# Kernel tuning notes

Hardware: AMD Instinct MI355X
Metric: run time of the kernel (lower is better)

## Reference

```python
import jax, jax.numpy as jnp
import numpy as np

N, D, E, TOPK = 8192, 2048, 8, 2

def setup_inputs() -> dict:
    key = jax.random.key(0)
    k1, k2, k3, k4 = jax.random.split(key, 4)
    inputs = jax.random.normal(k1, (N, D), dtype=jnp.float32)
    Wg = jax.random.normal(k2, (D, E), dtype=jnp.float32) * 0.02
    We = jax.random.normal(k3, (E, D, D), dtype=jnp.float32) * 0.02
    be = jax.random.normal(k4, (E, D), dtype=jnp.float32) * 0.02
    return {"inputs": inputs, "Wg": Wg, "We": We, "be": be}

def reference(inputs, Wg, We, be):
    # gate: [N, E] logits, top-k routing, softmax over the k selected logits (in fp32)
    gate_logits = inputs @ Wg                      # [N, E]
    topk_vals, selected = jax.lax.top_k(gate_logits, TOPK)  # [N, K], [N, K]
    weights = jax.nn.softmax(topk_vals.astype(jnp.float32), axis=1).astype(inputs.dtype)  # [N, K]

    results = jnp.zeros_like(inputs)
    for i in range(E):
        # combine weight for expert i per token (0 if not routed to i)
        coeff = jnp.sum(jnp.where(selected == i, weights, 0.0), axis=1)  # [N]
        expert_out = inputs @ We[i] + be[i]        # [N, D]
        results = results + coeff[:, None] * expert_out
    return results
```

## Files before the change

kernel.cpp:

```cpp
#include <hip/hip_runtime.h>
#include <stdint.h>

typedef unsigned short u16;
typedef __bf16 bf16x8 __attribute__((ext_vector_type(8)));
typedef float  f32x4  __attribute__((ext_vector_type(4)));

#define N_TOK 8192
#define DIM   2048
#define NEXP  8
#define RPAD  18432
#define NCHUNK 32
#define GT    576

#define OFF_CNT   0
#define OFF_HIST  1024
#define OFF_PRE   2048
#define OFF_RE    4096
#define OFF_RI    (OFF_RE + N_TOK * 8)
#define OFF_RW    (OFF_RI + N_TOK * 16)
#define OFF_TIDX  (OFF_RW + N_TOK * 8)
#define OFF_XB    (OFF_TIDX + NEXP * N_TOK * 4)
#define OFF_WT    (OFF_XB + (size_t)N_TOK * DIM * 2)
#define OFF_YP    (OFF_WT + (size_t)NEXP * DIM * DIM * 2)

__device__ __forceinline__ unsigned f2bf(float f) {
    unsigned int u = __float_as_uint(f);
    u = (u + 0x7FFFu + ((u >> 16) & 1u)) >> 16;
    return u;
}

__device__ __forceinline__ void gload16(const void* g, void* l) {
    __builtin_amdgcn_global_load_lds(
        (const __attribute__((address_space(1))) unsigned int*)g,
        (__attribute__((address_space(3))) unsigned int*)l,
        16, 0, 0);
}

__global__ __launch_bounds__(256) void k_gate(
    const float* __restrict__ x, const float* __restrict__ Wg,
    int2* __restrict__ route_e, float2* __restrict__ route_w,
    u16* __restrict__ Xb) {
    int wave = threadIdx.x >> 6, lane = threadIdx.x & 63;
    int n = blockIdx.x * 4 + wave;
    const float* xr = x + (size_t)n * DIM;
    u16* xbr = Xb + (size_t)n * DIM;
    double acc[8] = {0, 0, 0, 0, 0, 0, 0, 0};
#pragma unroll
    for (int it = 0; it < 4; it++) {
        int c = it * 512 + lane * 8;
        float4 a = *(const float4*)(xr + c);
        float4 b = *(const float4*)(xr + c + 4);
        uint4 o;
        o.x = f2bf(a.x) | (f2bf(a.y) << 16);
        o.y = f2bf(a.z) | (f2bf(a.w) << 16);
        o.z = f2bf(b.x) | (f2bf(b.y) << 16);
        o.w = f2bf(b.z) | (f2bf(b.w) << 16);
        *(uint4*)(xbr + c) = o;
        float xv[8] = {a.x, a.y, a.z, a.w, b.x, b.y, b.z, b.w};
        const float4* wp = (const float4*)(Wg + (size_t)c * 8);
#pragma unroll
        for (int j = 0; j < 8; j++) {
            float4 w0 = wp[j * 2], w1 = wp[j * 2 + 1];
            double xd = (double)xv[j];
            acc[0] += xd * (double)w0.x;
            acc[1] += xd * (double)w0.y;
            acc[2] += xd * (double)w0.z;
            acc[3] += xd * (double)w0.w;
            acc[4] += xd * (double)w1.x;
            acc[5] += xd * (double)w1.y;
            acc[6] += xd * (double)w1.z;
            acc[7] += xd * (double)w1.w;
        }
    }
#pragma unroll
    for (int off = 32; off; off >>= 1)
#pragma unroll
        for (int e = 0; e < 8; e++) acc[e] += __shfl_xor(acc[e], off);
    if (lane == 0) {
        float v[8];
#pragma unroll
        for (int e = 0; e < 8; e++) v[e] = (float)acc[e];
        int e0 = 0; float v0 = v[0];
#pragma unroll
        for (int e = 1; e < 8; e++) if (v[e] > v0) { v0 = v[e]; e0 = e; }
        int e1 = -1; float v1 = -1e30f;
#pragma unroll
        for (int e = 0; e < 8; e++) if (e != e0 && v[e] > v1) { v1 = v[e]; e1 = e; }
        float ex = expf(v1 - v0);
        route_e[n] = make_int2(e0, e1);
        route_w[n] = make_float2(1.0f / (1.0f + ex), ex / (1.0f + ex));
    }
}

__global__ __launch_bounds__(256) void k_hist(
    const int2* __restrict__ route_e, int* __restrict__ hist) {
    __shared__ int h[NEXP];
    int c = blockIdx.x, t = threadIdx.x;
    if (t < NEXP) h[t] = 0;
    __syncthreads();
    int2 re = route_e[c * 256 + t];
    atomicAdd(&h[re.x], 1);
    atomicAdd(&h[re.y], 1);
    __syncthreads();
    if (t < NEXP) hist[c * NEXP + t] = h[t];
}

__global__ void k_scan(const int* __restrict__ hist, int* __restrict__ pre,
                       int* __restrict__ cnt) {
    int e = threadIdx.x;
    if (e < NEXP) {
        int run = 0;
        for (int c = 0; c < NCHUNK; c++) { pre[c * NEXP + e] = run; run += hist[c * NEXP + e]; }
        cnt[e] = run;
    }
}

__global__ __launch_bounds__(256) void k_assign(
    const int2* __restrict__ route_e, const int* __restrict__ pre,
    int4* __restrict__ route_i, int* __restrict__ tok_idx) {
    __shared__ int wc0[4][NEXP], wc1[4][NEXP];
    int c = blockIdx.x, t = threadIdx.x, wave = t >> 6, lane = t & 63;
    int n = c * 256 + t;
    int2 re = route_e[n];
    unsigned long long lt = ((unsigned long long)1 << lane) - 1;
    int r0 = 0, r1 = 0;
#pragma unroll
    for (int e = 0; e < NEXP; e++) {
        unsigned long long m0 = __ballot(re.x == e);
        unsigned long long m1 = __ballot(re.y == e);
        if (lane == 0) { wc0[wave][e] = __popcll(m0); wc1[wave][e] = __popcll(m1); }
        if (re.x == e) r0 = __popcll(m0 & lt);
        if (re.y == e) r1 = __popcll(m1 & lt);
    }
    __syncthreads();
    int h0tot = 0;
#pragma unroll
    for (int w = 0; w < 4; w++) {
        if (w < wave) { r0 += wc0[w][re.x]; r1 += wc1[w][re.y]; }
        h0tot += wc0[w][re.y];
    }
    int p0 = pre[c * NEXP + re.x] + r0;
    int p1 = pre[c * NEXP + re.y] + h0tot + r1;
    route_i[n] = make_int4(re.x, re.y, p0, p1);
    tok_idx[re.x * N_TOK + p0] = n;
    tok_idx[re.y * N_TOK + p1] = n;
}

__global__ __launch_bounds__(256) void k_transpose_we(
    const float* __restrict__ We, u16* __restrict__ Wt) {
    __shared__ float t[64][65];
    int e = blockIdx.z, n0 = blockIdx.x * 64, k00 = blockIdx.y * 256;
    int tid = threadIdx.x;
    for (int kt = 0; kt < 4; kt++) {
        int k0 = k00 + kt * 64;
        const float* src = We + ((size_t)e * DIM + k0) * DIM + n0;
        if (kt) __syncthreads();
#pragma unroll
        for (int it = 0; it < 4; it++) {
            int item = it * 256 + tid;
            int r = item >> 4, c4 = (item & 15) * 4;
            float4 v = *(const float4*)(src + (size_t)r * DIM + c4);
            t[r][c4] = v.x; t[r][c4 + 1] = v.y; t[r][c4 + 2] = v.z; t[r][c4 + 3] = v.w;
        }
        __syncthreads();
        u16* dst = Wt + ((size_t)e * DIM + n0) * DIM + k0;
#pragma unroll
        for (int it = 0; it < 2; it++) {
            int item = it * 256 + tid;
            int nl = item >> 3, kc = (item & 7) * 8;
            unsigned m[8];
#pragma unroll
            for (int j = 0; j < 8; j++) m[j] = f2bf(t[kc + j][nl]);
            uint4 o;
            o.x = m[0] | (m[1] << 16); o.y = m[2] | (m[3] << 16);
            o.z = m[4] | (m[5] << 16); o.w = m[6] | (m[7] << 16);
            *(uint4*)(dst + (size_t)nl * DIM + kc) = o;
        }
    }
}

__global__ __launch_bounds__(512, 2) void k_moe_gemm(
    const u16* __restrict__ Xb, const u16* __restrict__ Wt,
    const float* __restrict__ be, const int* __restrict__ cnt,
    const int* __restrict__ tok_idx, u16* __restrict__ Yp) {
    extern __shared__ u16 lds[];

    int base[NEXP]; int pb = 0;
#pragma unroll
    for (int i = 0; i < NEXP; i++) { base[i] = pb; pb += ((cnt[i] + 255) >> 8) << 8; }

    int f = blockIdx.x;
    f = (f & 7) * (GT / 8) + (f >> 3);
    int m0 = (f >> 3) << 8, n0 = (f & 7) << 8;
    if (m0 >= pb) return;
    int e = 0;
#pragma unroll
    for (int i = 1; i < NEXP; i++) if (m0 >= base[i]) e = i;

    int tid = threadIdx.x, wave = tid >> 6, lane = tid & 63;
    int q = lane >> 4, mr = lane & 15;
    int wr = (wave >> 2) << 7;
    int wc = (wave & 3) << 6;

    const u16* pA[4]; const u16* pB[4];
#pragma unroll
    for (int j = 0; j < 4; j++) {
        int r = j * 64 + wave * 8 + (lane >> 3);
        int swz = ((lane & 7) ^ ((r >> 1) & 7)) << 3;
        int slot = m0 + r - base[e];
        int tok = tok_idx[e * N_TOK + slot] & (N_TOK - 1);
        pA[j] = Xb + (size_t)tok * DIM + swz;
        pB[j] = Wt + ((size_t)e * DIM + n0 + r) * DIM + swz;
    }

    u16* cA = lds;             u16* nA = lds + 16384;
    u16* cB = lds + 32768;     u16* nB = lds + 49152;
    int dofs = wave << 9;

    f32x4 acc[8][4] = {};

    gload16(pB[0], cB + 0     + dofs);
    gload16(pB[1], cB + 4096  + dofs);
    gload16(pA[0], cA + 0     + dofs);
    gload16(pA[2], cA + 8192  + dofs);
    gload16(pB[2], cB + 8192  + dofs);
    gload16(pB[3], cB + 12288 + dofs);
    gload16(pA[1], cA + 4096  + dofs);
    gload16(pA[3], cA + 12288 + dofs);
    asm volatile("s_waitcnt vmcnt(2)" ::: "memory");
    __builtin_amdgcn_s_barrier();
    __builtin_amdgcn_sched_barrier(0);

#pragma unroll 2
    for (int t = 0; t < 32; t++) {
        int koff = (t + 1 < 32 ? t + 1 : 31) << 6;
        gload16(pB[0] + koff, nB + 0     + dofs);
        gload16(pB[1] + koff, nB + 4096  + dofs);
        gload16(pA[0] + koff, nA + 0     + dofs);
        gload16(pA[2] + koff, nA + 8192  + dofs);
        bf16x8 b[4][2];
#pragma unroll
        for (int j = 0; j < 4; j++) {
            int R = wc + j * 16 + mr, sw = (R >> 1) & 7;
            b[j][0] = *(const bf16x8*)(cB + (R << 6) + (((0 + q) ^ sw) << 3));
            b[j][1] = *(const bf16x8*)(cB + (R << 6) + (((4 + q) ^ sw) << 3));
        }
        {
            bf16x8 a[2][2];
#pragma unroll
            for (int i2 = 0; i2 < 2; i2++) {
                int R = wr + i2 * 16 + mr, sw = (R >> 1) & 7;
                a[i2][0] = *(const bf16x8*)(cA + (R << 6) + (((0 + q) ^ sw) << 3));
                a[i2][1] = *(const bf16x8*)(cA + (R << 6) + (((4 + q) ^ sw) << 3));
            }
            __builtin_amdgcn_s_setprio(1);
#pragma unroll
            for (int kh = 0; kh < 2; kh++)
#pragma unroll
                for (int i2 = 0; i2 < 2; i2++)
#pragma unroll
                    for (int j = 0; j < 4; j++)
                        acc[i2][j] = __builtin_amdgcn_mfma_f32_16x16x32_bf16(
                            a[i2][kh], b[j][kh], acc[i2][j], 0, 0, 0);
            __builtin_amdgcn_s_setprio(0);
        }
        gload16(pB[2] + koff, nB + 8192  + dofs);
        gload16(pB[3] + koff, nB + 12288 + dofs);
        gload16(pA[1] + koff, nA + 4096  + dofs);
        gload16(pA[3] + koff, nA + 12288 + dofs);
        {
            bf16x8 a[2][2];
#pragma unroll
            for (int i2 = 0; i2 < 2; i2++) {
                int R = wr + 32 + i2 * 16 + mr, sw = (R >> 1) & 7;
                a[i2][0] = *(const bf16x8*)(cA + (R << 6) + (((0 + q) ^ sw) << 3));
                a[i2][1] = *(const bf16x8*)(cA + (R << 6) + (((4 + q) ^ sw) << 3));
            }
            __builtin_amdgcn_s_setprio(1);
#pragma unroll
            for (int kh = 0; kh < 2; kh++)
#pragma unroll
                for (int i2 = 0; i2 < 2; i2++)
#pragma unroll
                    for (int j = 0; j < 4; j++)
                        acc[2 + i2][j] = __builtin_amdgcn_mfma_f32_16x16x32_bf16(
                            a[i2][kh], b[j][kh], acc[2 + i2][j], 0, 0, 0);
            __builtin_amdgcn_s_setprio(0);
        }
        asm volatile("s_waitcnt vmcnt(8)" ::: "memory");
        __builtin_amdgcn_sched_barrier(0);
        __builtin_amdgcn_s_barrier();
        __builtin_amdgcn_sched_barrier(0);
        {
            bf16x8 a[2][2];
#pragma unroll
            for (int i2 = 0; i2 < 2; i2++) {
                int R = wr + 64 + i2 * 16 + mr, sw = (R >> 1) & 7;
                a[i2][0] = *(const bf16x8*)(cA + (R << 6) + (((0 + q) ^ sw) << 3));
                a[i2][1] = *(const bf16x8*)(cA + (R << 6) + (((4 + q) ^ sw) << 3));
            }
            __builtin_amdgcn_s_setprio(1);
#pragma unroll
            for (int kh = 0; kh < 2; kh++)
#pragma unroll
                for (int i2 = 0; i2 < 2; i2++)
#pragma unroll
                    for (int j = 0; j < 4; j++)
                        acc[4 + i2][j] = __builtin_amdgcn_mfma_f32_16x16x32_bf16(
                            a[i2][kh], b[j][kh], acc[4 + i2][j], 0, 0, 0);
            __builtin_amdgcn_s_setprio(0);
        }
        {
            bf16x8 a[2][2];
#pragma unroll
            for (int i2 = 0; i2 < 2; i2++) {
                int R = wr + 96 + i2 * 16 + mr, sw = (R >> 1) & 7;
                a[i2][0] = *(const bf16x8*)(cA + (R << 6) + (((0 + q) ^ sw) << 3));
                a[i2][1] = *(const bf16x8*)(cA + (R << 6) + (((4 + q) ^ sw) << 3));
            }
            __builtin_amdgcn_s_setprio(1);
#pragma unroll
            for (int kh = 0; kh < 2; kh++)
#pragma unroll
                for (int i2 = 0; i2 < 2; i2++)
#pragma unroll
                    for (int j = 0; j < 4; j++)
                        acc[6 + i2][j] = __builtin_amdgcn_mfma_f32_16x16x32_bf16(
                            a[i2][kh], b[j][kh], acc[6 + i2][j], 0, 0, 0);
            __builtin_amdgcn_s_setprio(0);
        }
        asm volatile("s_waitcnt vmcnt(2)" ::: "memory");
        __builtin_amdgcn_sched_barrier(0);
        __builtin_amdgcn_s_barrier();
        __builtin_amdgcn_sched_barrier(0);
        u16* tp;
        tp = cA; cA = nA; nA = tp;
        tp = cB; cB = nB; nB = tp;
    }
    asm volatile("s_waitcnt vmcnt(0)" ::: "memory");

    float bev[4];
#pragma unroll
    for (int j = 0; j < 4; j++) bev[j] = be[e * DIM + n0 + wc + j * 16 + mr];
#pragma unroll
    for (int i = 0; i < 8; i++) {
#pragma unroll
        for (int r = 0; r < 4; r++) {
            int row = wr + i * 16 + q * 4 + r;
            u16* yrow = Yp + (size_t)(m0 + row) * DIM + n0 + wc + mr;
#pragma unroll
            for (int j = 0; j < 4; j++)
                yrow[j * 16] = (u16)f2bf(acc[i][j][r] + bev[j]);
        }
    }
}

__global__ __launch_bounds__(256) void k_combine(
    const u16* __restrict__ Yp, const int* __restrict__ cnt,
    const int4* __restrict__ route_i, const float2* __restrict__ route_w,
    float* __restrict__ out) {
    int base[NEXP]; int pb = 0;
#pragma unroll
    for (int i = 0; i < NEXP; i++) { base[i] = pb; pb += ((cnt[i] + 255) >> 8) << 8; }
    int n = blockIdx.x, tid = threadIdx.x;
    int4 ri = route_i[n]; float2 w = route_w[n];
    size_t r0 = (size_t)base[ri.x] + ri.z;
    size_t r1 = (size_t)base[ri.y] + ri.w;
    uint4 ya = ((const uint4*)(Yp + r0 * DIM))[tid];
    uint4 yb = ((const uint4*)(Yp + r1 * DIM))[tid];
    float4 o0, o1;
    unsigned a, b;
    a = ya.x; b = yb.x;
    o0.x = w.x * __uint_as_float(a << 16) + w.y * __uint_as_float(b << 16);
    o0.y = w.x * __uint_as_float(a & 0xffff0000u) + w.y * __uint_as_float(b & 0xffff0000u);
    a = ya.y; b = yb.y;
    o0.z = w.x * __uint_as_float(a << 16) + w.y * __uint_as_float(b << 16);
    o0.w = w.x * __uint_as_float(a & 0xffff0000u) + w.y * __uint_as_float(b & 0xffff0000u);
    a = ya.z; b = yb.z;
    o1.x = w.x * __uint_as_float(a << 16) + w.y * __uint_as_float(b << 16);
    o1.y = w.x * __uint_as_float(a & 0xffff0000u) + w.y * __uint_as_float(b & 0xffff0000u);
    a = ya.w; b = yb.w;
    o1.z = w.x * __uint_as_float(a << 16) + w.y * __uint_as_float(b << 16);
    o1.w = w.x * __uint_as_float(a & 0xffff0000u) + w.y * __uint_as_float(b & 0xffff0000u);
    float4* op = (float4*)(out + (size_t)n * DIM) + tid * 2;
    op[0] = o0; op[1] = o1;
}

extern "C" void kernel_launch(void* const* d_in, const int* in_sizes, int n_in,
                              void* d_out, int out_size, void* d_ws, size_t ws_size,
                              hipStream_t stream) {
    const float* x  = (const float*)d_in[0];
    const float* Wg = (const float*)d_in[1];
    const float* We = (const float*)d_in[2];
    const float* be = (const float*)d_in[3];
    float* out = (float*)d_out;
    char* ws = (char*)d_ws;
    int*    cnt     = (int*)(ws + OFF_CNT);
    int*    hist    = (int*)(ws + OFF_HIST);
    int*    pre     = (int*)(ws + OFF_PRE);
    int2*   route_e = (int2*)(ws + OFF_RE);
    int4*   route_i = (int4*)(ws + OFF_RI);
    float2* route_w = (float2*)(ws + OFF_RW);
    int*    tok_idx = (int*)(ws + OFF_TIDX);
    u16*    Xb      = (u16*)(ws + OFF_XB);
    u16*    Wt      = (u16*)(ws + OFF_WT);
    u16*    Yp      = (u16*)(ws + OFF_YP);

    static int g_attr_done = 0;
    if (!g_attr_done) {
        (void)hipFuncSetAttribute((const void*)k_moe_gemm,
                                  hipFuncAttributeMaxDynamicSharedMemorySize,
                                  131072);
        g_attr_done = 1;
    }

    k_gate<<<N_TOK / 4, 256, 0, stream>>>(x, Wg, route_e, route_w, Xb);
    k_hist<<<NCHUNK, 256, 0, stream>>>(route_e, hist);
    k_scan<<<1, 64, 0, stream>>>(hist, pre, cnt);
    k_assign<<<NCHUNK, 256, 0, stream>>>(route_e, pre, route_i, tok_idx);
    k_transpose_we<<<dim3(DIM / 64, DIM / 256, NEXP), 256, 0, stream>>>(We, Wt);
    k_moe_gemm<<<dim3(GT), 512, 131072, stream>>>(Xb, Wt, be, cnt, tok_idx, Yp);
    k_combine<<<N_TOK, 256, 0, stream>>>(Yp, cnt, route_i, route_w, out);
}
```

Before: 499.5 us.

## Split-K the tail wave of MoE GEMM tiles and reduce partials in combine

The first 512 GEMM tiles keep the full K loop. The remaining 64 tail tiles are split eight ways along K into short blocks that write fp32 partial sums to a scratch buffer. The combine kernel sums those partials and adds the bias for rows in the tail region. The aim is to remove the under-filled final wave of GEMM blocks, at the cost of extra fp32 scratch traffic and a larger combine read.

```diff
diff --git a/kernel.cpp b/kernel.cpp
--- a/kernel.cpp
+++ b/kernel.cpp
@@ -10,7 +10,8 @@
 #define NEXP  8
 #define RPAD  18432
 #define NCHUNK 32
-#define GT    576
+#define NFULL 512
+#define NTAIL 64
 
 #define OFF_CNT   0
 #define OFF_HIST  1024
@@ -22,6 +23,7 @@
 #define OFF_XB    (OFF_TIDX + NEXP * N_TOK * 4)
 #define OFF_WT    (OFF_XB + (size_t)N_TOK * DIM * 2)
 #define OFF_YP    (OFF_WT + (size_t)NEXP * DIM * DIM * 2)
+#define OFF_YS    (OFF_YP + (size_t)RPAD * DIM * 2)
 
 __device__ __forceinline__ unsigned f2bf(float f) {
     unsigned int u = __float_as_uint(f);
@@ -182,15 +184,26 @@
 __global__ __launch_bounds__(512, 2) void k_moe_gemm(
     const u16* __restrict__ Xb, const u16* __restrict__ Wt,
     const float* __restrict__ be, const int* __restrict__ cnt,
-    const int* __restrict__ tok_idx, u16* __restrict__ Yp) {
+    const int* __restrict__ tok_idx, u16* __restrict__ Yp,
+    float* __restrict__ Ys) {
     extern __shared__ u16 lds[];
 
     int base[NEXP]; int pb = 0;
 #pragma unroll
     for (int i = 0; i < NEXP; i++) { base[i] = pb; pb += ((cnt[i] + 255) >> 8) << 8; }
 
-    int f = blockIdx.x;
-    f = (f & 7) * (GT / 8) + (f >> 3);
+    int bid = blockIdx.x;
+    int f, tb, tn;
+    float* ysc = nullptr;
+    if (bid < NFULL) {
+        f = (bid & 7) * (NFULL / 8) + (bid >> 3);
+        tb = 0; tn = 32;
+    } else {
+        int i8 = (bid - NFULL) >> 3, k8 = (bid - NFULL) & 7;
+        f = NFULL + i8;
+        tb = k8 * 4; tn = 4;
+        ysc = Ys + ((size_t)i8 * 8 + k8) * 65536;
+    }
     int m0 = (f >> 3) << 8, n0 = (f & 7) << 8;
     if (m0 >= pb) return;
     int e = 0;
@@ -209,8 +222,8 @@
         int swz = ((lane & 7) ^ ((r >> 1) & 7)) << 3;
         int slot = m0 + r - base[e];
         int tok = tok_idx[e * N_TOK + slot] & (N_TOK - 1);
-        pA[j] = Xb + (size_t)tok * DIM + swz;
-        pB[j] = Wt + ((size_t)e * DIM + n0 + r) * DIM + swz;
+        pA[j] = Xb + (size_t)tok * DIM + swz + (tb << 6);
+        pB[j] = Wt + ((size_t)e * DIM + n0 + r) * DIM + swz + (tb << 6);
     }
 
     u16* cA = lds;             u16* nA = lds + 16384;
@@ -232,8 +245,8 @@
     __builtin_amdgcn_sched_barrier(0);
 
 #pragma unroll 2
-    for (int t = 0; t < 32; t++) {
-        int koff = (t + 1 < 32 ? t + 1 : 31) << 6;
+    for (int t = 0; t < tn; t++) {
+        int koff = (t + 1 < tn ? t + 1 : tn - 1) << 6;
         gload16(pB[0] + koff, nB + 0     + dofs);
         gload16(pB[1] + koff, nB + 4096  + dofs);
         gload16(pA[0] + koff, nA + 0     + dofs);
@@ -339,24 +352,39 @@
     }
     asm volatile("s_waitcnt vmcnt(0)" ::: "memory");
 
-    float bev[4];
-#pragma unroll
-    for (int j = 0; j < 4; j++) bev[j] = be[e * DIM + n0 + wc + j * 16 + mr];
-#pragma unroll
-    for (int i = 0; i < 8; i++) {
-#pragma unroll
-        for (int r = 0; r < 4; r++) {
-            int row = wr + i * 16 + q * 4 + r;
-            u16* yrow = Yp + (size_t)(m0 + row) * DIM + n0 + wc + mr;
-#pragma unroll
-            for (int j = 0; j < 4; j++)
-                yrow[j * 16] = (u16)f2bf(acc[i][j][r] + bev[j]);
+    if (bid < NFULL) {
+        float bev[4];
+#pragma unroll
+        for (int j = 0; j < 4; j++) bev[j] = be[e * DIM + n0 + wc + j * 16 + mr];
+#pragma unroll
+        for (int i = 0; i < 8; i++) {
+#pragma unroll
+            for (int r = 0; r < 4; r++) {
+                int row = wr + i * 16 + q * 4 + r;
+                u16* yrow = Yp + (size_t)(m0 + row) * DIM + n0 + wc + mr;
+#pragma unroll
+                for (int j = 0; j < 4; j++)
+                    yrow[j * 16] = (u16)f2bf(acc[i][j][r] + bev[j]);
+            }
+        }
+    } else {
+#pragma unroll
+        for (int i = 0; i < 8; i++) {
+#pragma unroll
+            for (int r = 0; r < 4; r++) {
+                int row = wr + i * 16 + q * 4 + r;
+                float* yo = ysc + (size_t)row * 256 + wc + mr;
+#pragma unroll
+                for (int j = 0; j < 4; j++)
+                    yo[j * 16] = acc[i][j][r];
+            }
         }
     }
 }
 
 __global__ __launch_bounds__(256) void k_combine(
-    const u16* __restrict__ Yp, const int* __restrict__ cnt,
+    const u16* __restrict__ Yp, const float* __restrict__ Ys,
+    const float* __restrict__ be, const int* __restrict__ cnt,
     const int4* __restrict__ route_i, const float2* __restrict__ route_w,
     float* __restrict__ out) {
     int base[NEXP]; int pb = 0;
@@ -366,22 +394,46 @@
     int4 ri = route_i[n]; float2 w = route_w[n];
     size_t r0 = (size_t)base[ri.x] + ri.z;
     size_t r1 = (size_t)base[ri.y] + ri.w;
-    uint4 ya = ((const uint4*)(Yp + r0 * DIM))[tid];
-    uint4 yb = ((const uint4*)(Yp + r1 * DIM))[tid];
+    int c0 = tid * 8;
+    float y0[8], y1[8];
+#pragma unroll
+    for (int side = 0; side < 2; side++) {
+        size_t r = side ? r1 : r0;
+        int ex = side ? ri.y : ri.x;
+        float* y = side ? y1 : y0;
+        if (r < (size_t)(NFULL * 32)) {
+            uint4 ya = ((const uint4*)(Yp + r * DIM))[tid];
+            unsigned v[4] = {ya.x, ya.y, ya.z, ya.w};
+#pragma unroll
+            for (int k = 0; k < 4; k++) {
+                y[2 * k]     = __uint_as_float(v[k] << 16);
+                y[2 * k + 1] = __uint_as_float(v[k] & 0xffff0000u);
+            }
+        } else {
+            int i8 = ((int)(r >> 8) - 64) * 8 + (c0 >> 8);
+            const float* p = Ys + (size_t)i8 * 8 * 65536
+                             + (size_t)((int)(r & 255) * 256 + (c0 & 255));
+            float s[8] = {0, 0, 0, 0, 0, 0, 0, 0};
+#pragma unroll
+            for (int k8 = 0; k8 < 8; k8++) {
+                float4 u0 = *(const float4*)(p + (size_t)k8 * 65536);
+                float4 u1 = *(const float4*)(p + (size_t)k8 * 65536 + 4);
+                s[0] += u0.x; s[1] += u0.y; s[2] += u0.z; s[3] += u0.w;
+                s[4] += u1.x; s[5] += u1.y; s[6] += u1.z; s[7] += u1.w;
+            }
+#pragma unroll
+            for (int k = 0; k < 8; k++) y[k] = s[k] + be[ex * DIM + c0 + k];
+        }
+    }
     float4 o0, o1;
-    unsigned a, b;
-    a = ya.x; b = yb.x;
-    o0.x = w.x * __uint_as_float(a << 16) + w.y * __uint_as_float(b << 16);
-    o0.y = w.x * __uint_as_float(a & 0xffff0000u) + w.y * __uint_as_float(b & 0xffff0000u);
-    a = ya.y; b = yb.y;
-    o0.z = w.x * __uint_as_float(a << 16) + w.y * __uint_as_float(b << 16);
-    o0.w = w.x * __uint_as_float(a & 0xffff0000u) + w.y * __uint_as_float(b & 0xffff0000u);
-    a = ya.z; b = yb.z;
-    o1.x = w.x * __uint_as_float(a << 16) + w.y * __uint_as_float(b << 16);
-    o1.y = w.x * __uint_as_float(a & 0xffff0000u) + w.y * __uint_as_float(b & 0xffff0000u);
-    a = ya.w; b = yb.w;
-    o1.z = w.x * __uint_as_float(a << 16) + w.y * __uint_as_float(b << 16);
-    o1.w = w.x * __uint_as_float(a & 0xffff0000u) + w.y * __uint_as_float(b & 0xffff0000u);
+    o0.x = w.x * y0[0] + w.y * y1[0];
+    o0.y = w.x * y0[1] + w.y * y1[1];
+    o0.z = w.x * y0[2] + w.y * y1[2];
+    o0.w = w.x * y0[3] + w.y * y1[3];
+    o1.x = w.x * y0[4] + w.y * y1[4];
+    o1.y = w.x * y0[5] + w.y * y1[5];
+    o1.z = w.x * y0[6] + w.y * y1[6];
+    o1.w = w.x * y0[7] + w.y * y1[7];
     float4* op = (float4*)(out + (size_t)n * DIM) + tid * 2;
     op[0] = o0; op[1] = o1;
 }
@@ -405,6 +457,7 @@
     u16*    Xb      = (u16*)(ws + OFF_XB);
     u16*    Wt      = (u16*)(ws + OFF_WT);
     u16*    Yp      = (u16*)(ws + OFF_YP);
+    float*  Ys      = (float*)(ws + OFF_YS);
 
     static int g_attr_done = 0;
     if (!g_attr_done) {
@@ -419,6 +472,7 @@
     k_scan<<<1, 64, 0, stream>>>(hist, pre, cnt);
     k_assign<<<NCHUNK, 256, 0, stream>>>(route_e, pre, route_i, tok_idx);
     k_transpose_we<<<dim3(DIM / 64, DIM / 256, NEXP), 256, 0, stream>>>(We, Wt);
-    k_moe_gemm<<<dim3(GT), 512, 131072, stream>>>(Xb, Wt, be, cnt, tok_idx, Yp);
-    k_combine<<<N_TOK, 256, 0, stream>>>(Yp, cnt, route_i, route_w, out);
-}
+    k_moe_gemm<<<dim3(NFULL + NTAIL * 8), 512, 131072, stream>>>(
+        Xb, Wt, be, cnt, tok_idx, Yp, Ys);
+    k_combine<<<N_TOK, 256, 0, stream>>>(Yp, Ys, be, cnt, route_i, route_w, out);
+}
```

Measured after the change: 483.4 us. -3.2%, faster.
